# Performance work log

Measured on AMD Instinct MI355X. Metric: run time of the kernel, lower is better.

Reference implementation:

```python
import jax, jax.numpy as jnp
import numpy as np

# Model constants (hard-coded latent/embed sizes in the torch module)
NP = 16          # n_patch
C, H, W = 3, 256, 256
B = 256
PH, PW = H // NP, W // NP
D = C * PH * PW  # 768 patch feature dim
L = 64           # latent_size
E = 32           # embeded_size
NM = 3           # n_msa (hard-coded)
EPS = 1e-5


def layernorm(x, s, b):
    m = jnp.mean(x, axis=-1, keepdims=True)
    v = jnp.mean(jnp.square(x - m), axis=-1, keepdims=True)
    return (x - m) / jnp.sqrt(v + EPS) * s + b


def setup_inputs() -> dict:
    key = jax.random.key(0)
    ks = jax.random.split(key, 16)
    rn = lambda k, shape: jax.random.normal(k, shape, jnp.float32) * 0.02
    return {
        "x": jax.random.normal(ks[0], (B, C, H, W), jnp.float32),
        "in_ln_s": jnp.ones((D,), jnp.float32), "in_ln_b": jnp.zeros((D,), jnp.float32),
        "in_W": rn(ks[1], (D, L)), "in_b": jnp.zeros((L,), jnp.float32),
        "in_ln2_s": jnp.ones((L,), jnp.float32), "in_ln2_b": jnp.zeros((L,), jnp.float32),
        "msa_ln_s": jnp.ones((NM, L), jnp.float32), "msa_ln_b": jnp.zeros((NM, L), jnp.float32),
        "Wq": rn(ks[2], (NM, L, E)), "bq": jnp.zeros((NM, E), jnp.float32),
        "Wk": rn(ks[3], (NM, L, E)), "bk": jnp.zeros((NM, E), jnp.float32),
        "Wv": rn(ks[4], (NM, L, E)), "bv": jnp.zeros((NM, E), jnp.float32),
        "mhp_W1": rn(ks[5], (NM * E, L)), "mhp_b1": jnp.zeros((L,), jnp.float32),
        "mhp_W2": rn(ks[6], (L, L)), "mhp_b2": jnp.zeros((L,), jnp.float32),
        "mlp_ln_s": jnp.ones((L,), jnp.float32), "mlp_ln_b": jnp.zeros((L,), jnp.float32),
        "mlp_W1": rn(ks[7], (L, L)), "mlp_b1": jnp.zeros((L,), jnp.float32),
        "mlp_W2": rn(ks[8], (L, L)), "mlp_b2": jnp.zeros((L,), jnp.float32),
        "mlp_W3": rn(ks[9], (L, L)), "mlp_b3": jnp.zeros((L,), jnp.float32),
        "mlp_W4": rn(ks[10], (L, L)), "mlp_b4": jnp.zeros((L,), jnp.float32),
        "out_W": rn(ks[11], (NP * NP * L, 1)), "out_b": jnp.zeros((1,), jnp.float32),
    }


def reference(x, in_ln_s, in_ln_b, in_W, in_b, in_ln2_s, in_ln2_b,
              msa_ln_s, msa_ln_b, Wq, bq, Wk, bk, Wv, bv,
              mhp_W1, mhp_b1, mhp_W2, mhp_b2,
              mlp_ln_s, mlp_ln_b, mlp_W1, mlp_b1, mlp_W2, mlp_b2,
              mlp_W3, mlp_b3, mlp_W4, mlp_b4, out_W, out_b):
    b_, c_, h_, w_ = x.shape
    ph, pw = h_ // NP, w_ // NP
    # 'b c (h p0) (w p1) -> b (p0 p1) (c h w)'
    t = x.reshape(b_, c_, ph, NP, pw, NP).transpose(0, 3, 5, 1, 2, 4)
    t = t.reshape(b_, NP * NP, c_ * ph * pw)
    t = layernorm(t, in_ln_s, in_ln_b)
    t = t @ in_W + in_b
    t = layernorm(t, in_ln2_s, in_ln2_b)  # x_skip: [B, S, L]

    def one_msa(ln_s, ln_b, wq, bq_, wk, bk_, wv, bv_):
        xn = layernorm(t, ln_s, ln_b)
        q = xn @ wq + bq_
        k = xn @ wk + bk_
        v = xn @ wv + bv_
        a = jax.nn.softmax(jnp.einsum('bse,bte->bst', q, k), axis=-1)  # no 1/sqrt(d) scaling (faithful)
        return a @ v  # [B, S, E]  (dropout is train=False -> identity)

    heads = jax.vmap(one_msa)(msa_ln_s, msa_ln_b, Wq, bq, Wk, bk, Wv, bv)  # [NM, B, S, E]
    cat = jnp.transpose(heads, (1, 2, 0, 3)).reshape(b_, NP * NP, NM * E)

    h = (cat @ mhp_W1 + mhp_b1) @ mhp_W2 + mhp_b2
    x_skip = h + t

    m = layernorm(x_skip, mlp_ln_s, mlp_ln_b)
    m = m @ mlp_W1 + mlp_b1
    m = m @ mlp_W2 + mlp_b2
    m = jax.nn.gelu(m, approximate=False)
    m = m @ mlp_W3 + mlp_b3
    m = m @ mlp_W4 + mlp_b4
    out = (m + x_skip).reshape(b_, -1)
    return out @ out_W + out_b  # [B, 1]
```

## Files before the change

kernel.cpp:

```cpp
#include <hip/hip_runtime.h>
#include <math.h>

typedef __attribute__((ext_vector_type(8))) short short8;
typedef __attribute__((ext_vector_type(4))) short short4v;
typedef __attribute__((ext_vector_type(4))) float f32x4;
typedef __attribute__((ext_vector_type(2))) float f32x2;

#define DEV static __device__ __forceinline__

DEV unsigned short f2b(float f){
  union{float f; unsigned u;} x; x.f = f;
  unsigned r = (x.u + 0x7fffu + ((x.u>>16)&1u))>>16;
  return (unsigned short)r;
}

#define MFMA(a,b,c) __builtin_amdgcn_mfma_f32_16x16x32_bf16((a),(b),(c),0,0,0)

DEV void prep_one(int id,
    const float* inW, const float* Wq, const float* Wk, const float* Wv,
    const float* m1, const float* m2,
    const float* p1, const float* p2, const float* p3, const float* p4,
    const float* mss, const float* mls, const float* msb,
    const float* bq, const float* bk, const float* bv,
    const float* mlb, const float* mb1,
    unsigned short* wsw, float* qkvb, float* mlpb1)
{
  if(id < 94208){
    const float* src; int NT, base; int harg = -1, w1flag = 0;
    if      (id < 49152){ src=inW; NT=4; base=0; }
    else if (id < 67584){ int r=id-49152; int slab=r>>11; int h=slab/3, m=slab-h*3;
                          src=(m==0?Wq:(m==1?Wk:Wv))+h*2048; NT=2; base=49152+slab*2048; harg=h; }
    else if (id < 73728){ src=m1; NT=4; base=67584; }
    else if (id < 77824){ src=m2; NT=4; base=73728; }
    else if (id < 81920){ src=p1; NT=4; base=77824; w1flag=1; }
    else if (id < 86016){ src=p2; NT=4; base=81920; }
    else if (id < 90112){ src=p3; NT=4; base=86016; }
    else                { src=p4; NT=4; base=90112; }
    int o = id - base;
    int j = o&7, l = (o>>3)&63, rest = o>>9;
    int nt = rest % NT, kc = rest / NT;
    int k = kc*32 + ((l>>4)<<3) + j;
    int n = nt*16 + (l&15);
    float scale = 1.f;
    if(harg >= 0) scale = mss[harg*64 + k];
    if(w1flag)    scale = mls[k];
    wsw[id] = f2b(src[k*(NT*16) + n] * scale);
  } else if(id < 94496){
    int o = id - 94208;
    int h = o/96, m = (o - h*96)/32, e = o&31;
    const float* W  = (m==0?Wq:(m==1?Wk:Wv)) + h*2048;
    const float* bb = (m==0?bq:(m==1?bk:bv));
    float s = 0.f;
    for(int l=0;l<64;++l) s += msb[h*64+l]*W[l*32+e];
    qkvb[o] = s + bb[h*32+e];
  } else if(id < 94560){
    int n = id - 94496;
    float s = 0.f;
    for(int l=0;l<64;++l) s += mlb[l]*p1[l*64+n];
    mlpb1[n] = s + mb1[n];
  }
}

__global__ __launch_bounds__(256) void kprep(
    const float* __restrict__ inW, unsigned short* __restrict__ wsw)
{
  int id = blockIdx.x*256 + threadIdx.x;
  int o = id;
  int j = o&7, l = (o>>3)&63, rest = o>>9;
  int nt = rest & 3, kc = rest >> 2;
  int k = kc*32 + ((l>>4)<<3) + j;
  int n = nt*16 + (l&15);
  wsw[id] = f2b(inW[k*64 + n]);
}

__global__ __launch_bounds__(256) void k1_patch(
    const float* __restrict__ x,
    const float* __restrict__ ln1s, const float* __restrict__ ln1b,
    unsigned short* __restrict__ wsw, const float* __restrict__ inb,
    const float* __restrict__ ln2s, const float* __restrict__ ln2b,
    float* __restrict__ xskip, unsigned short* __restrict__ zf,
    const float* __restrict__ inW,
    const float* __restrict__ Wq, const float* __restrict__ Wk,
    const float* __restrict__ Wv,
    const float* __restrict__ m1, const float* __restrict__ m2,
    const float* __restrict__ p1, const float* __restrict__ p2,
    const float* __restrict__ p3, const float* __restrict__ p4,
    const float* __restrict__ mss, const float* __restrict__ mls,
    const float* __restrict__ msb,
    const float* __restrict__ bq, const float* __restrict__ bk,
    const float* __restrict__ bv,
    const float* __restrict__ mlb, const float* __restrict__ mb1,
    float* __restrict__ qkvb, float* __restrict__ mlpb1)
{
  const int tid = threadIdx.x;
  const int bp = blockIdx.x;
  if(bp >= 4096){
    int id = 49152 + (bp - 4096)*256 + tid;
    prep_one(id, inW, Wq, Wk, Wv, m1, m2, p1, p2, p3, p4,
             mss, mls, msb, bq, bk, bv, mlb, mb1, wsw, qkvb, mlpb1);
    return;
  }
  __shared__ unsigned short Tf[24*64*8];
  __shared__ float Cbuf[16][68];
  __shared__ float wstat[4][16][2];
  const int lane = tid & 63, wv = tid >> 6;
  const int b = bp >> 4, p0 = bp & 15;
  const int a = lane & 3;

  const float* xb = x + (size_t)b * (3*256*256);
  f32x4 rv[12];
  float sum[4] = {0.f,0.f,0.f,0.f}, ssq[4] = {0.f,0.f,0.f,0.f};
#pragma unroll
  for(int it=0; it<12; ++it){
    int rr = it*4 + wv;
    int c = rr >> 4, i = rr & 15;
    rv[it] = *(const f32x4*)&xb[(size_t)(c*256 + i*16 + p0)*256 + lane*4];
#pragma unroll
    for(int u=0; u<4; ++u){ float v = rv[it][u]; sum[u] += v; ssq[u] += v*v; }
  }
#pragma unroll
  for(int u=0; u<4; ++u){
    sum[u] += __shfl_xor(sum[u],4);  ssq[u] += __shfl_xor(ssq[u],4);
    sum[u] += __shfl_xor(sum[u],8);  ssq[u] += __shfl_xor(ssq[u],8);
    sum[u] += __shfl_xor(sum[u],16); ssq[u] += __shfl_xor(ssq[u],16);
    sum[u] += __shfl_xor(sum[u],32); ssq[u] += __shfl_xor(ssq[u],32);
  }
  if(lane < 4){
#pragma unroll
    for(int u=0; u<4; ++u){
      wstat[wv][lane*4+u][0] = sum[u];
      wstat[wv][lane*4+u][1] = ssq[u];
    }
  }
  __syncthreads();
  float mean[4], rstd[4];
#pragma unroll
  for(int u=0; u<4; ++u){
    int pv = a*4 + u;
    float ts = wstat[0][pv][0]+wstat[1][pv][0]+wstat[2][pv][0]+wstat[3][pv][0];
    float tq = wstat[0][pv][1]+wstat[1][pv][1]+wstat[2][pv][1]+wstat[3][pv][1];
    mean[u] = ts * (1.f/768.f);
    rstd[u] = rsqrtf(tq*(1.f/768.f) - mean[u]*mean[u] + 1e-5f);
  }
#pragma unroll
  for(int it=0; it<12; ++it){
    int rr = it*4 + wv;
    int c = rr >> 4, i = rr & 15, j = lane >> 2;
    int d = c*256 + i*16 + j;
    float ls = ln1s[d], lb = ln1b[d];
    int tb = ((d>>5)*64 + ((d&31)>>3)*16)*8 + (d&7);
#pragma unroll
    for(int u=0; u<4; ++u){
      float xv = (rv[it][u]-mean[u])*rstd[u]*ls + lb;
      Tf[ tb + (a*4+u)*8 ] = f2b(xv);
    }
  }
  __syncthreads();

  f32x4 acc = {0.f,0.f,0.f,0.f};
  const short8* wf = (const short8*)wsw;
#pragma unroll
  for(int kc=0; kc<24; ++kc){
    short8 aa = *(const short8*)&Tf[(kc*64 + lane)*8];
    short8 bb = wf[(kc*4 + wv)*64 + lane];
    acc = MFMA(aa, bb, acc);
  }
  const int c15 = lane & 15, rg = lane >> 4;
  float bias = inb[wv*16 + c15];
#pragma unroll
  for(int r=0; r<4; ++r) Cbuf[rg*4+r][wv*16+c15] = acc[r] + bias;
  __syncthreads();

  {
    int row = tid >> 4, cq = (tid & 15) * 4;
    float v0=Cbuf[row][cq+0], v1=Cbuf[row][cq+1], v2=Cbuf[row][cq+2], v3=Cbuf[row][cq+3];
    float s = v0+v1+v2+v3;
    float q = v0*v0+v1*v1+v2*v2+v3*v3;
    s += __shfl_xor(s,1); s += __shfl_xor(s,2); s += __shfl_xor(s,4); s += __shfl_xor(s,8);
    q += __shfl_xor(q,1); q += __shfl_xor(q,2); q += __shfl_xor(q,4); q += __shfl_xor(q,8);
    float m2  = s*(1.f/64.f);
    float rs2 = rsqrtf(q*(1.f/64.f) - m2*m2 + 1e-5f);
    f32x4 o;
    o[0] = (v0-m2)*rs2*ln2s[cq+0] + ln2b[cq+0];
    o[1] = (v1-m2)*rs2*ln2s[cq+1] + ln2b[cq+1];
    o[2] = (v2-m2)*rs2*ln2s[cq+2] + ln2b[cq+2];
    o[3] = (v3-m2)*rs2*ln2s[cq+3] + ln2b[cq+3];
    int grow = b*256 + p0*16 + row;
    *(f32x4*)&xskip[ (size_t)grow*64 + cq ] = o;
    float s2 = o[0]+o[1]+o[2]+o[3];
    float q2 = o[0]*o[0]+o[1]*o[1]+o[2]*o[2]+o[3]*o[3];
    s2 += __shfl_xor(s2,1); s2 += __shfl_xor(s2,2); s2 += __shfl_xor(s2,4); s2 += __shfl_xor(s2,8);
    q2 += __shfl_xor(q2,1); q2 += __shfl_xor(q2,2); q2 += __shfl_xor(q2,4); q2 += __shfl_xor(q2,8);
    float mm  = s2*(1.f/64.f);
    float rr2 = rsqrtf(q2*(1.f/64.f) - mm*mm + 1e-5f);
    short4v zz;
    zz[0] = (short)f2b((o[0]-mm)*rr2);
    zz[1] = (short)f2b((o[1]-mm)*rr2);
    zz[2] = (short)f2b((o[2]-mm)*rr2);
    zz[3] = (short)f2b((o[3]-mm)*rr2);
    int fi = (p0*2 + (cq>>5))*512 + ((cq&31)>>3)*128 + row*8 + (cq&7);
    *(short4v*)&zf[ (size_t)b*16384 + fi ] = zz;
  }
}

__global__ __launch_bounds__(256) void kA_attn(
    const unsigned short* __restrict__ zf,
    const unsigned short* __restrict__ wsw, const float* __restrict__ qkvb,
    unsigned short* __restrict__ catg)
{
  __shared__ unsigned short Kf[8192];
  __shared__ unsigned short Vf[8192];
  __shared__ unsigned short scr[4][1024];
  const int tid = threadIdx.x, lane = tid&63, wv = tid>>6;
  const int c15 = lane&15, rg = lane>>4;
  const int id = blockIdx.x, b = id/3, h = id - b*3;
  const short8* zg = (const short8*)(zf + (size_t)b*16384);
  const short8* wf = ((const short8*)(wsw + 49152)) + h*3*256;
  unsigned short* sw = scr[wv];
  float be[6];
#pragma unroll
  for(int i=0;i<6;++i) be[i] = qkvb[(h*3 + (i>>1))*32 + (i&1)*16 + c15];

  short8 aq[4];
#pragma unroll
  for(int si=0; si<4; ++si){
    const int st = wv + si*4;
    short8 a0 = zg[(st*2+0)*64 + lane];
    short8 a1 = zg[(st*2+1)*64 + lane];
#pragma unroll
    for(int mat=0; mat<3; ++mat){
#pragma unroll
      for(int et=0; et<2; ++et){
        f32x4 acc = {0.f,0.f,0.f,0.f};
        acc = MFMA(a0, wf[mat*256 + et*64 + lane], acc);
        acc = MFMA(a1, wf[mat*256 + (2+et)*64 + lane], acc);
        float bias = be[mat*2+et];
#pragma unroll
        for(int r=0;r<4;++r){
          unsigned short val = f2b(acc[r] + bias);
          int s15 = rg*4 + r;
          if(mat==0){
            sw[ ((et*2 + (c15>>3))*16 + s15)*8 + (c15&7) ] = val;
          } else if(mat==1){
            Kf[ (st*64 + (et*2 + (c15>>3))*16 + s15)*8 + (c15&7) ] = val;
          } else {
            int s = st*16 + s15;
            Vf[ (((s>>5)*2 + et)*64 + ((s&31)>>3)*16 + c15)*8 + (s&7) ] = val;
          }
        }
      }
      if(mat==0) aq[si] = ((const short8*)sw)[lane];
    }
  }
  __syncthreads();

  const f32x4 z4 = {0.f,0.f,0.f,0.f};
#pragma unroll
  for(int si=0; si<4; ++si){
    const int st = wv + si*4;
    f32x4 sc[16];
#pragma unroll
    for(int tt=0; tt<16; ++tt) sc[tt] = MFMA(aq[si], ((const short8*)Kf)[tt*64 + lane], z4);
    float mx[4], sm[4];
#pragma unroll
    for(int r=0; r<4; ++r){
      float m = sc[0][r];
#pragma unroll
      for(int tt=1; tt<16; ++tt) m = fmaxf(m, sc[tt][r]);
      m = fmaxf(m, __shfl_xor(m,1)); m = fmaxf(m, __shfl_xor(m,2));
      m = fmaxf(m, __shfl_xor(m,4)); m = fmaxf(m, __shfl_xor(m,8));
      mx[r] = m; sm[r] = 0.f;
    }
#pragma unroll
    for(int tt=0; tt<16; ++tt)
#pragma unroll
      for(int r=0; r<4; ++r){
        float e = __expf(sc[tt][r] - mx[r]);
        sc[tt][r] = e; sm[r] += e;
      }
#pragma unroll
    for(int r=0; r<4; ++r){
      float s = sm[r];
      s += __shfl_xor(s,1); s += __shfl_xor(s,2); s += __shfl_xor(s,4); s += __shfl_xor(s,8);
      sm[r] = 1.f / s;
    }
    f32x4 o0 = z4, o1 = z4;
#pragma unroll
    for(int kc=0; kc<8; ++kc){
#pragma unroll
      for(int t2=0; t2<2; ++t2){
        int tt = kc*2 + t2;
        int tbr = t2*16 + c15;
#pragma unroll
        for(int r=0; r<4; ++r)
          sw[ (((tbr>>3)*16 + rg*4 + r)<<3) + (tbr&7) ] = f2b(sc[tt][r] * sm[r]);
      }
      short8 pa = ((const short8*)sw)[lane];
      o0 = MFMA(pa, ((const short8*)Vf)[(kc*2+0)*64 + lane], o0);
      o1 = MFMA(pa, ((const short8*)Vf)[(kc*2+1)*64 + lane], o1);
    }
    {
      size_t cb = (size_t)(b*4 + (st>>2))*6144 + (st&3)*1536 + h*512;
#pragma unroll
      for(int r=0; r<4; ++r){
        int fi = (c15>>3)*128 + (rg*4+r)*8 + (c15&7);
        catg[cb + fi]       = f2b(o0[r]);
        catg[cb + 256 + fi] = f2b(o1[r]);
      }
    }
  }
}

__global__ __launch_bounds__(256) void kB_tail(
    const unsigned short* __restrict__ catg, const float* __restrict__ xskip,
    const unsigned short* __restrict__ w1f, const float* __restrict__ b1,
    const unsigned short* __restrict__ w2f, const float* __restrict__ b2,
    const unsigned short* __restrict__ p1f, const float* __restrict__ p1b,
    const unsigned short* __restrict__ p2f, const float* __restrict__ pb2,
    const unsigned short* __restrict__ p3f, const float* __restrict__ pb3,
    const unsigned short* __restrict__ p4f, const float* __restrict__ pb4,
    const float* __restrict__ outw, float* __restrict__ part)
{
  __shared__ unsigned short catf[6144];
  __shared__ unsigned short fa[4096];
  __shared__ unsigned short fb[4096];
  __shared__ float rstat[4][64][2];
  __shared__ float red[4];
  const int tid = threadIdx.x, lane = tid&63, wv = tid>>6;
  const int c15 = lane&15, rg = lane>>4;
  const int bid = blockIdx.x, b = bid>>2, sg = bid&3;
  {
    const unsigned short* cg = catg + (size_t)bid*6144;
#pragma unroll
    for(int it=0; it<3; ++it){
      int o = it*2048 + tid*8;
      *(short8*)&catf[o] = *(const short8*)&cg[o];
    }
  }
  __syncthreads();
  const short8* w1 = (const short8*)w1f;
  const short8* w2 = (const short8*)w2f;
  const short8* q1 = (const short8*)p1f;
  const short8* q2 = (const short8*)p2f;
  const short8* q3 = (const short8*)p3f;
  const short8* q4 = (const short8*)p4f;
  const int kch = wv>>1, gw = (wv&1)*2 + (c15>>3), jw = c15&7;
  {
    float bb = b1[wv*16+c15];
#pragma unroll
    for(int st=0; st<4; ++st){
      f32x4 a = {0.f,0.f,0.f,0.f};
#pragma unroll
      for(int kc=0; kc<3; ++kc)
        a = MFMA(*(const short8*)&catf[((st*3+kc)*64+lane)*8], w1[(kc*4+wv)*64+lane], a);
#pragma unroll
      for(int r=0; r<4; ++r)
        fa[ (((st*2+kch)*64 + gw*16 + rg*4 + r)<<3) + jw ] = f2b(a[r] + bb);
    }
  }
  __syncthreads();
  f32x4 xs2[4];
  const float* xr = xskip + (size_t)(b*256 + sg*64)*64;
  {
    float bb = b2[wv*16+c15];
#pragma unroll
    for(int st=0; st<4; ++st){
      f32x4 a = {0.f,0.f,0.f,0.f};
#pragma unroll
      for(int kc=0; kc<2; ++kc)
        a = MFMA(*(const short8*)&fa[((st*2+kc)*64+lane)*8], w2[(kc*4+wv)*64+lane], a);
#pragma unroll
      for(int r=0; r<4; ++r)
        xs2[st][r] = a[r] + bb + xr[(st*16 + rg*4 + r)*64 + wv*16 + c15];
    }
  }
#pragma unroll
  for(int st=0; st<4; ++st)
#pragma unroll
    for(int r=0; r<4; ++r){
      float sv = xs2[st][r], qv = sv*sv;
      sv += __shfl_xor(sv,1); sv += __shfl_xor(sv,2); sv += __shfl_xor(sv,4); sv += __shfl_xor(sv,8);
      qv += __shfl_xor(qv,1); qv += __shfl_xor(qv,2); qv += __shfl_xor(qv,4); qv += __shfl_xor(qv,8);
      if(c15==0){ int row = st*16+rg*4+r; rstat[wv][row][0]=sv; rstat[wv][row][1]=qv; }
    }
  __syncthreads();
#pragma unroll
  for(int st=0; st<4; ++st)
#pragma unroll
    for(int r=0; r<4; ++r){
      int row = st*16+rg*4+r;
      float tsu = rstat[0][row][0]+rstat[1][row][0]+rstat[2][row][0]+rstat[3][row][0];
      float tqu = rstat[0][row][1]+rstat[1][row][1]+rstat[2][row][1]+rstat[3][row][1];
      float mean = tsu*(1.f/64.f);
      float rstd = rsqrtf(tqu*(1.f/64.f) - mean*mean + 1e-5f);
      fa[ (((st*2+kch)*64 + gw*16 + (row&15))<<3) + jw ] = f2b((xs2[st][r]-mean)*rstd);
    }
  __syncthreads();
  {
    float bb = p1b[wv*16+c15];
#pragma unroll
    for(int st=0; st<4; ++st){
      f32x4 a = {0.f,0.f,0.f,0.f};
#pragma unroll
      for(int kc=0; kc<2; ++kc)
        a = MFMA(*(const short8*)&fa[((st*2+kc)*64+lane)*8], q1[(kc*4+wv)*64+lane], a);
#pragma unroll
      for(int r=0; r<4; ++r)
        fb[ (((st*2+kch)*64 + gw*16 + rg*4 + r)<<3) + jw ] = f2b(a[r] + bb);
    }
  }
  __syncthreads();
  {
    float bb = pb2[wv*16+c15];
#pragma unroll
    for(int st=0; st<4; ++st){
      f32x4 a = {0.f,0.f,0.f,0.f};
#pragma unroll
      for(int kc=0; kc<2; ++kc)
        a = MFMA(*(const short8*)&fb[((st*2+kc)*64+lane)*8], q2[(kc*4+wv)*64+lane], a);
#pragma unroll
      for(int r=0; r<4; ++r){
        float v = a[r] + bb;
        v = 0.5f*v*(1.f + erff(v*0.70710678118654752440f));
        fa[ (((st*2+kch)*64 + gw*16 + rg*4 + r)<<3) + jw ] = f2b(v);
      }
    }
  }
  __syncthreads();
  {
    float bb = pb3[wv*16+c15];
#pragma unroll
    for(int st=0; st<4; ++st){
      f32x4 a = {0.f,0.f,0.f,0.f};
#pragma unroll
      for(int kc=0; kc<2; ++kc)
        a = MFMA(*(const short8*)&fa[((st*2+kc)*64+lane)*8], q3[(kc*4+wv)*64+lane], a);
#pragma unroll
      for(int r=0; r<4; ++r)
        fb[ (((st*2+kch)*64 + gw*16 + rg*4 + r)<<3) + jw ] = f2b(a[r] + bb);
    }
  }
  __syncthreads();
  {
    float bb = pb4[wv*16+c15];
    float partial = 0.f;
#pragma unroll
    for(int st=0; st<4; ++st){
      f32x4 a = {0.f,0.f,0.f,0.f};
#pragma unroll
      for(int kc=0; kc<2; ++kc)
        a = MFMA(*(const short8*)&fb[((st*2+kc)*64+lane)*8], q4[(kc*4+wv)*64+lane], a);
#pragma unroll
      for(int r=0; r<4; ++r){
        int row = st*16 + rg*4 + r;
        float v = a[r] + bb + xs2[st][r];
        partial += v * outw[(sg*64 + row)*64 + wv*16 + c15];
      }
    }
    partial += __shfl_xor(partial,1); partial += __shfl_xor(partial,2);
    partial += __shfl_xor(partial,4); partial += __shfl_xor(partial,8);
    partial += __shfl_xor(partial,16); partial += __shfl_xor(partial,32);
    if(lane==0) red[wv] = partial;
    __syncthreads();
    if(tid==0) part[bid] = red[0]+red[1]+red[2]+red[3];
  }
}

__global__ void k5_out(const float* __restrict__ part, const float* __restrict__ outb,
                       float* __restrict__ out){
  int b = threadIdx.x;
  out[b] = part[b*4] + part[b*4+1] + part[b*4+2] + part[b*4+3] + outb[0];
}

extern "C" void kernel_launch(void* const* d_in, const int* in_sizes, int n_in,
                              void* d_out, int out_size, void* d_ws, size_t ws_size,
                              hipStream_t stream)
{
  const float* x    = (const float*)d_in[0];
  const float* ln1s = (const float*)d_in[1];
  const float* ln1b = (const float*)d_in[2];
  const float* inW  = (const float*)d_in[3];
  const float* inb  = (const float*)d_in[4];
  const float* ln2s = (const float*)d_in[5];
  const float* ln2b = (const float*)d_in[6];
  const float* mss  = (const float*)d_in[7];
  const float* msb  = (const float*)d_in[8];
  const float* Wq   = (const float*)d_in[9];
  const float* bq   = (const float*)d_in[10];
  const float* Wk   = (const float*)d_in[11];
  const float* bk   = (const float*)d_in[12];
  const float* Wv   = (const float*)d_in[13];
  const float* bv   = (const float*)d_in[14];
  const float* mhW1 = (const float*)d_in[15];
  const float* mhb1 = (const float*)d_in[16];
  const float* mhW2 = (const float*)d_in[17];
  const float* mhb2 = (const float*)d_in[18];
  const float* mls  = (const float*)d_in[19];
  const float* mlb  = (const float*)d_in[20];
  const float* mW1  = (const float*)d_in[21];
  const float* mb1  = (const float*)d_in[22];
  const float* mW2  = (const float*)d_in[23];
  const float* mb2  = (const float*)d_in[24];
  const float* mW3  = (const float*)d_in[25];
  const float* mb3  = (const float*)d_in[26];
  const float* mW4  = (const float*)d_in[27];
  const float* mb4  = (const float*)d_in[28];
  const float* outW = (const float*)d_in[29];
  const float* outb = (const float*)d_in[30];
  (void)in_sizes; (void)n_in; (void)out_size;

  char* ws = (char*)d_ws;
  float*          xskip = (float*)         (ws + 0);
  unsigned short* catg  = (unsigned short*)(ws + 16777216);
  unsigned short* wsw   = (unsigned short*)(ws + 29360128);
  unsigned short* zf    = (unsigned short*)(ws + 29548544);
  float*          qkvb  = (float*)         (ws + 37937152);
  float*          mlpb1 = (float*)         (ws + 37938304);
  float*          part  = (float*)         (ws + 37938560);
  if(ws_size < 37942656u) return;

  float* out = (float*)d_out;

  kprep<<<dim3(192), dim3(256), 0, stream>>>(inW, wsw);
  k1_patch<<<dim3(4096 + 178), dim3(256), 0, stream>>>(x, ln1s, ln1b, wsw, inb,
      ln2s, ln2b, xskip, zf,
      inW, Wq, Wk, Wv, mhW1, mhW2, mW1, mW2, mW3, mW4,
      mss, mls, msb, bq, bk, bv, mlb, mb1, qkvb, mlpb1);
  kA_attn<<<dim3(768), dim3(256), 0, stream>>>(zf, wsw, qkvb, catg);
  kB_tail<<<dim3(1024), dim3(256), 0, stream>>>(catg, xskip,
      wsw + 67584, mhb1, wsw + 73728, mhb2,
      wsw + 77824, mlpb1, wsw + 81920, mb2, wsw + 86016, mb3, wsw + 90112, mb4,
      outW, part);
  k5_out<<<dim3(1), dim3(256), 0, stream>>>(part, outb, out);
}
```

Before: 98.09 us.

## Make tail kernel wave-private: each wave owns 16 rows, drop block barriers

Restructures the MLP tail kernel so each wave processes its own 16 rows across all 64 output columns, instead of splitting output columns across waves. Activations are exchanged only through a small per-wave LDS scratch, and the layernorm statistics are reduced with intra-wave shuffles. This removes most __syncthreads and the cross-wave rstat reduction, and loads the cat tile straight from global into registers. In exchange each wave now reads all four weight column tiles, and the per-wave scratch reuse relies on in-wave ordering of LDS writes and reads.

```diff
diff --git a/kernel.cpp b/kernel.cpp
--- a/kernel.cpp
+++ b/kernel.cpp
@@ -321,149 +321,127 @@
     const unsigned short* __restrict__ p4f, const float* __restrict__ pb4,
     const float* __restrict__ outw, float* __restrict__ part)
 {
-  __shared__ unsigned short catf[6144];
-  __shared__ unsigned short fa[4096];
-  __shared__ unsigned short fb[4096];
-  __shared__ float rstat[4][64][2];
+  __shared__ unsigned short scr[4][1024];
   __shared__ float red[4];
   const int tid = threadIdx.x, lane = tid&63, wv = tid>>6;
   const int c15 = lane&15, rg = lane>>4;
   const int bid = blockIdx.x, b = bid>>2, sg = bid&3;
-  {
-    const unsigned short* cg = catg + (size_t)bid*6144;
-#pragma unroll
-    for(int it=0; it<3; ++it){
-      int o = it*2048 + tid*8;
-      *(short8*)&catf[o] = *(const short8*)&cg[o];
-    }
-  }
-  __syncthreads();
+  unsigned short* sw = scr[wv];
   const short8* w1 = (const short8*)w1f;
   const short8* w2 = (const short8*)w2f;
   const short8* q1 = (const short8*)p1f;
   const short8* q2 = (const short8*)p2f;
   const short8* q3 = (const short8*)p3f;
   const short8* q4 = (const short8*)p4f;
-  const int kch = wv>>1, gw = (wv&1)*2 + (c15>>3), jw = c15&7;
-  {
-    float bb = b1[wv*16+c15];
-#pragma unroll
-    for(int st=0; st<4; ++st){
-      f32x4 a = {0.f,0.f,0.f,0.f};
-#pragma unroll
-      for(int kc=0; kc<3; ++kc)
-        a = MFMA(*(const short8*)&catf[((st*3+kc)*64+lane)*8], w1[(kc*4+wv)*64+lane], a);
-#pragma unroll
-      for(int r=0; r<4; ++r)
-        fa[ (((st*2+kch)*64 + gw*16 + rg*4 + r)<<3) + jw ] = f2b(a[r] + bb);
-    }
-  }
+  const f32x4 z4 = {0.f,0.f,0.f,0.f};
+  const int slot_base = (c15>>3)*128 + rg*32 + (c15&7);
+
+  const short8* cg = (const short8*)(catg + (size_t)bid*6144 + wv*1536);
+  short8 ac0 = cg[lane], ac1 = cg[64+lane], ac2 = cg[128+lane];
+
+  short8 a0, a1;
+  {
+#pragma unroll
+    for(int nt=0; nt<4; ++nt){
+      f32x4 acc = MFMA(ac0, w1[(0*4+nt)*64+lane], z4);
+      acc = MFMA(ac1, w1[(1*4+nt)*64+lane], acc);
+      acc = MFMA(ac2, w1[(2*4+nt)*64+lane], acc);
+      float bb = b1[nt*16+c15];
+#pragma unroll
+      for(int r=0;r<4;++r)
+        sw[ (nt>>1)*512 + (nt&1)*256 + slot_base + r*8 ] = f2b(acc[r]+bb);
+    }
+    a0 = ((const short8*)sw)[lane]; a1 = ((const short8*)sw)[64+lane];
+  }
+  f32x4 xs2[4];
+  const float* xr = xskip + (size_t)(b*256 + sg*64 + wv*16)*64;
+  {
+#pragma unroll
+    for(int nt=0; nt<4; ++nt){
+      f32x4 acc = MFMA(a0, w2[(0*4+nt)*64+lane], z4);
+      acc = MFMA(a1, w2[(1*4+nt)*64+lane], acc);
+      float bb = b2[nt*16+c15];
+#pragma unroll
+      for(int r=0;r<4;++r)
+        xs2[nt][r] = acc[r] + bb + xr[(rg*4+r)*64 + nt*16 + c15];
+    }
+  }
+  {
+#pragma unroll
+    for(int r=0;r<4;++r){
+      float s = xs2[0][r]+xs2[1][r]+xs2[2][r]+xs2[3][r];
+      float q = xs2[0][r]*xs2[0][r]+xs2[1][r]*xs2[1][r]
+              + xs2[2][r]*xs2[2][r]+xs2[3][r]*xs2[3][r];
+      s += __shfl_xor(s,1); s += __shfl_xor(s,2); s += __shfl_xor(s,4); s += __shfl_xor(s,8);
+      q += __shfl_xor(q,1); q += __shfl_xor(q,2); q += __shfl_xor(q,4); q += __shfl_xor(q,8);
+      float mean = s*(1.f/64.f);
+      float rstd = rsqrtf(q*(1.f/64.f) - mean*mean + 1e-5f);
+#pragma unroll
+      for(int nt=0;nt<4;++nt)
+        sw[ (nt>>1)*512 + (nt&1)*256 + slot_base + r*8 ] = f2b((xs2[nt][r]-mean)*rstd);
+    }
+    a0 = ((const short8*)sw)[lane]; a1 = ((const short8*)sw)[64+lane];
+  }
+  {
+#pragma unroll
+    for(int nt=0; nt<4; ++nt){
+      f32x4 acc = MFMA(a0, q1[(0*4+nt)*64+lane], z4);
+      acc = MFMA(a1, q1[(1*4+nt)*64+lane], acc);
+      float bb = p1b[nt*16+c15];
+#pragma unroll
+      for(int r=0;r<4;++r)
+        sw[ (nt>>1)*512 + (nt&1)*256 + slot_base + r*8 ] = f2b(acc[r]+bb);
+    }
+    a0 = ((const short8*)sw)[lane]; a1 = ((const short8*)sw)[64+lane];
+  }
+  {
+#pragma unroll
+    for(int nt=0; nt<4; ++nt){
+      f32x4 acc = MFMA(a0, q2[(0*4+nt)*64+lane], z4);
+      acc = MFMA(a1, q2[(1*4+nt)*64+lane], acc);
+      float bb = pb2[nt*16+c15];
+#pragma unroll
+      for(int r=0;r<4;++r){
+        float v = acc[r] + bb;
+        v = 0.5f*v*(1.f + erff(v*0.70710678118654752440f));
+        sw[ (nt>>1)*512 + (nt&1)*256 + slot_base + r*8 ] = f2b(v);
+      }
+    }
+    a0 = ((const short8*)sw)[lane]; a1 = ((const short8*)sw)[64+lane];
+  }
+  {
+#pragma unroll
+    for(int nt=0; nt<4; ++nt){
+      f32x4 acc = MFMA(a0, q3[(0*4+nt)*64+lane], z4);
+      acc = MFMA(a1, q3[(1*4+nt)*64+lane], acc);
+      float bb = pb3[nt*16+c15];
+#pragma unroll
+      for(int r=0;r<4;++r)
+        sw[ (nt>>1)*512 + (nt&1)*256 + slot_base + r*8 ] = f2b(acc[r]+bb);
+    }
+    a0 = ((const short8*)sw)[lane]; a1 = ((const short8*)sw)[64+lane];
+  }
+  float partial = 0.f;
+  {
+    const float* ow = outw + (sg*64 + wv*16)*64;
+#pragma unroll
+    for(int nt=0; nt<4; ++nt){
+      f32x4 acc = MFMA(a0, q4[(0*4+nt)*64+lane], z4);
+      acc = MFMA(a1, q4[(1*4+nt)*64+lane], acc);
+      float bb = pb4[nt*16+c15];
+#pragma unroll
+      for(int r=0;r<4;++r){
+        float v = acc[r] + bb + xs2[nt][r];
+        partial += v * ow[(rg*4+r)*64 + nt*16 + c15];
+      }
+    }
+  }
+  partial += __shfl_xor(partial,1); partial += __shfl_xor(partial,2);
+  partial += __shfl_xor(partial,4); partial += __shfl_xor(partial,8);
+  partial += __shfl_xor(partial,16); partial += __shfl_xor(partial,32);
+  if(lane==0) red[wv] = partial;
   __syncthreads();
-  f32x4 xs2[4];
-  const float* xr = xskip + (size_t)(b*256 + sg*64)*64;
-  {
-    float bb = b2[wv*16+c15];
-#pragma unroll
-    for(int st=0; st<4; ++st){
-      f32x4 a = {0.f,0.f,0.f,0.f};
-#pragma unroll
-      for(int kc=0; kc<2; ++kc)
-        a = MFMA(*(const short8*)&fa[((st*2+kc)*64+lane)*8], w2[(kc*4+wv)*64+lane], a);
-#pragma unroll
-      for(int r=0; r<4; ++r)
-        xs2[st][r] = a[r] + bb + xr[(st*16 + rg*4 + r)*64 + wv*16 + c15];
-    }
-  }
-#pragma unroll
-  for(int st=0; st<4; ++st)
-#pragma unroll
-    for(int r=0; r<4; ++r){
-      float sv = xs2[st][r], qv = sv*sv;
-      sv += __shfl_xor(sv,1); sv += __shfl_xor(sv,2); sv += __shfl_xor(sv,4); sv += __shfl_xor(sv,8);
-      qv += __shfl_xor(qv,1); qv += __shfl_xor(qv,2); qv += __shfl_xor(qv,4); qv += __shfl_xor(qv,8);
-      if(c15==0){ int row = st*16+rg*4+r; rstat[wv][row][0]=sv; rstat[wv][row][1]=qv; }
-    }
-  __syncthreads();
-#pragma unroll
-  for(int st=0; st<4; ++st)
-#pragma unroll
-    for(int r=0; r<4; ++r){
-      int row = st*16+rg*4+r;
-      float tsu = rstat[0][row][0]+rstat[1][row][0]+rstat[2][row][0]+rstat[3][row][0];
-      float tqu = rstat[0][row][1]+rstat[1][row][1]+rstat[2][row][1]+rstat[3][row][1];
-      float mean = tsu*(1.f/64.f);
-      float rstd = rsqrtf(tqu*(1.f/64.f) - mean*mean + 1e-5f);
-      fa[ (((st*2+kch)*64 + gw*16 + (row&15))<<3) + jw ] = f2b((xs2[st][r]-mean)*rstd);
-    }
-  __syncthreads();
-  {
-    float bb = p1b[wv*16+c15];
-#pragma unroll
-    for(int st=0; st<4; ++st){
-      f32x4 a = {0.f,0.f,0.f,0.f};
-#pragma unroll
-      for(int kc=0; kc<2; ++kc)
-        a = MFMA(*(const short8*)&fa[((st*2+kc)*64+lane)*8], q1[(kc*4+wv)*64+lane], a);
-#pragma unroll
-      for(int r=0; r<4; ++r)
-        fb[ (((st*2+kch)*64 + gw*16 + rg*4 + r)<<3) + jw ] = f2b(a[r] + bb);
-    }
-  }
-  __syncthreads();
-  {
-    float bb = pb2[wv*16+c15];
-#pragma unroll
-    for(int st=0; st<4; ++st){
-      f32x4 a = {0.f,0.f,0.f,0.f};
-#pragma unroll
-      for(int kc=0; kc<2; ++kc)
-        a = MFMA(*(const short8*)&fb[((st*2+kc)*64+lane)*8], q2[(kc*4+wv)*64+lane], a);
-#pragma unroll
-      for(int r=0; r<4; ++r){
-        float v = a[r] + bb;
-        v = 0.5f*v*(1.f + erff(v*0.70710678118654752440f));
-        fa[ (((st*2+kch)*64 + gw*16 + rg*4 + r)<<3) + jw ] = f2b(v);
-      }
-    }
-  }
-  __syncthreads();
-  {
-    float bb = pb3[wv*16+c15];
-#pragma unroll
-    for(int st=0; st<4; ++st){
-      f32x4 a = {0.f,0.f,0.f,0.f};
-#pragma unroll
-      for(int kc=0; kc<2; ++kc)
-        a = MFMA(*(const short8*)&fa[((st*2+kc)*64+lane)*8], q3[(kc*4+wv)*64+lane], a);
-#pragma unroll
-      for(int r=0; r<4; ++r)
-        fb[ (((st*2+kch)*64 + gw*16 + rg*4 + r)<<3) + jw ] = f2b(a[r] + bb);
-    }
-  }
-  __syncthreads();
-  {
-    float bb = pb4[wv*16+c15];
-    float partial = 0.f;
-#pragma unroll
-    for(int st=0; st<4; ++st){
-      f32x4 a = {0.f,0.f,0.f,0.f};
-#pragma unroll
-      for(int kc=0; kc<2; ++kc)
-        a = MFMA(*(const short8*)&fb[((st*2+kc)*64+lane)*8], q4[(kc*4+wv)*64+lane], a);
-#pragma unroll
-      for(int r=0; r<4; ++r){
-        int row = st*16 + rg*4 + r;
-        float v = a[r] + bb + xs2[st][r];
-        partial += v * outw[(sg*64 + row)*64 + wv*16 + c15];
-      }
-    }
-    partial += __shfl_xor(partial,1); partial += __shfl_xor(partial,2);
-    partial += __shfl_xor(partial,4); partial += __shfl_xor(partial,8);
-    partial += __shfl_xor(partial,16); partial += __shfl_xor(partial,32);
-    if(lane==0) red[wv] = partial;
-    __syncthreads();
-    if(tid==0) part[bid] = red[0]+red[1]+red[2]+red[3];
-  }
+  if(tid==0) part[bid] = red[0]+red[1]+red[2]+red[3];
 }
 
 __global__ void k5_out(const float* __restrict__ part, const float* __restrict__ outb,
```

Result: faster. 93.85 us (-4.3%).
